# Performance work log

Measured on AMD Instinct MI355X. Metric: run time of the kernel, lower is better.

## Reference

```python
import jax, jax.numpy as jnp
import numpy as np

H = 1024
B, LK, LQ = 16, 2048, 64


def setup_inputs() -> dict:
    key0 = jax.random.key(0)
    ks = jax.random.split(key0, 16)
    f = jax.random.normal
    return {
        "query": f(ks[0], (B, 1, H), jnp.float32),
        "key": f(ks[1], (B, LK, 2 * H), jnp.float32),
        "value": f(ks[2], (B, LK, 2 * H), jnp.float32),
        "mask": jax.random.randint(ks[3], (B, 1, LK), 0, 2).astype(jnp.int32),
        "q_key": f(ks[4], (B, LQ, 2 * H), jnp.float32),
        "q_value": f(ks[5], (B, LQ, 2 * H), jnp.float32),
        "q_mask": jax.random.randint(ks[6], (B, 1, LQ), 0, 2).astype(jnp.int32),
        "alphas_state": jax.random.uniform(ks[7], (B, 1, LK), jnp.float32),
        "q_alphas_state": jax.random.uniform(ks[8], (B, 1, LQ), jnp.float32),
        # nn.Linear params: W is [out, in], y = x @ W.T + b
        "W_q": f(ks[9], (2 * H, H + 2 * H + 1), jnp.float32) * 0.02,
        "b_q": jnp.zeros((2 * H,), jnp.float32),
        "W_t": f(ks[10], (2 * H, H + 2 * H + 1 + 2 * H), jnp.float32) * 0.02,
        "b_t": jnp.zeros((2 * H,), jnp.float32),
        "query_other": jax.random.uniform(ks[11], (1, 2 * H), jnp.float32, minval=-0.005, maxval=0.005),
        "text_other": jax.random.uniform(ks[12], (1, 2 * H), jnp.float32, minval=-0.005, maxval=0.005),
    }


def reference(query, key, value, mask, q_key, q_value, q_mask,
              alphas_state, q_alphas_state,
              W_q, b_q, W_t, b_t, query_other, text_other):
    neg_inf = jnp.float32(-jnp.inf)
    Bq, Lq, _ = q_key.shape
    Bk, Lk, _ = key.shape
    # ---- query-side additive attention ----
    qrep = jnp.broadcast_to(query, (Bq, Lq, query.shape[-1]))            # repeat(1, Lq, 1)
    feat = jnp.concatenate([q_key, qrep, q_alphas_state.reshape(Bq, Lq, 1)], axis=-1)
    h = jnp.tanh(jnp.einsum('bli,oi->blo', feat, W_q) + b_q)             # [B, Lq, 2H]
    scores = jnp.einsum('blo,o->bl', h, query_other[0])[:, None, :]      # fused per-batch loop -> [B,1,Lq]
    scores = jnp.where(q_mask == 0, neg_inf, scores)
    q_alphas = jax.nn.softmax(scores, axis=-1)
    query_loss = jnp.sum(jnp.min(
        jnp.concatenate([q_alphas_state[:, 0, :], q_alphas[:, 0, :]], axis=0), axis=0))
    q_context = jnp.einsum('bql,bld->bqd', q_alphas, q_value)            # bmm -> [B,1,2H]
    # ---- text-side additive attention ----
    qrep_k = jnp.broadcast_to(query, (Bk, Lk, query.shape[-1]))
    ctx_rep = jnp.broadcast_to(q_context, (Bk, Lk, q_context.shape[-1]))
    feat_t = jnp.concatenate([key, qrep_k, alphas_state.reshape(Bk, Lk, 1), ctx_rep], axis=-1)
    h_t = jnp.tanh(jnp.einsum('bli,oi->blo', feat_t, W_t) + b_t)         # [B, Lk, 2H]
    scores_t = jnp.einsum('blo,o->bl', h_t, text_other[0])[:, None, :]   # [B,1,Lk]
    scores_t = jnp.where(mask == 0, neg_inf, scores_t)
    alphas = jax.nn.softmax(scores_t, axis=-1)
    text_loss = jnp.sum(jnp.min(
        jnp.concatenate([alphas_state[:, 0, :], alphas[:, 0, :]], axis=0), axis=0))
    context = jnp.einsum('bql,bld->bqd', alphas, value)                  # [B,1,2H]
    return (context, alphas, q_alphas, text_loss, query_loss)
```

## Files before the change

### kernel.cpp

```cpp
#include <hip/hip_runtime.h>
#include <hip/hip_bf16.h>
#include <math.h>

#define GK 2048
#define NCB 16

typedef __attribute__((ext_vector_type(8))) short bf16x8;
typedef __attribute__((ext_vector_type(4))) float f32x4;
typedef __attribute__((ext_vector_type(4))) float f4v;
typedef __attribute__((ext_vector_type(4))) unsigned short u16x4;
typedef __attribute__((ext_vector_type(8))) unsigned short u16x8;

__device__ __forceinline__ unsigned short f2bf(float x) {
    unsigned int u = __float_as_uint(x);
    u += 0x7fffu + ((u >> 16) & 1u);
    return (unsigned short)(u >> 16);
}

__device__ __forceinline__ void gl_lds16(const void* g, void* l) {
    __builtin_amdgcn_global_load_lds(
        (const __attribute__((address_space(1))) unsigned int*)g,
        (__attribute__((address_space(3))) unsigned int*)l, 16, 0, 0);
}

__global__ void prep_kernel(const float* __restrict__ Wt, const float* __restrict__ Wq,
                            const float* __restrict__ q_key, const float* __restrict__ key,
                            const float* __restrict__ query, const float* __restrict__ b_q,
                            unsigned short* __restrict__ Wtk, unsigned short* __restrict__ Wqk,
                            unsigned short* __restrict__ qkb, unsigned short* __restrict__ keyb,
                            float* __restrict__ w3q, float* __restrict__ w3t,
                            float* __restrict__ Dq) {
    int b = blockIdx.x, tid = threadIdx.x;
    if (b < 32768) {
        long i = ((long)b << 11) + (tid << 3);
        f4v a = *(const f4v*)(key + i);
        f4v c = *(const f4v*)(key + i + 4);
        u16x8 r;
        r[0] = f2bf(a[0]); r[1] = f2bf(a[1]); r[2] = f2bf(a[2]); r[3] = f2bf(a[3]);
        r[4] = f2bf(c[0]); r[5] = f2bf(c[1]); r[6] = f2bf(c[2]); r[7] = f2bf(c[3]);
        *(u16x8*)(keyb + i) = r;
        return;
    }
    int b2 = b - 32768;
    if (b2 < 2048) {
        const float* s = Wt + (size_t)b2 * 5121;
        unsigned short* d = Wtk + (size_t)b2 * 2048;
#pragma unroll
        for (int k = 0; k < 8; k++) { int c = tid + (k << 8); d[c] = f2bf(s[c]); }
    } else if (b2 < 4096) {
        int o = b2 - 2048;
        const float* s = Wq + (size_t)o * 3073;
        unsigned short* d = Wqk + (size_t)o * 2048;
#pragma unroll
        for (int k = 0; k < 8; k++) { int c = tid + (k << 8); d[c] = f2bf(s[c]); }
    } else if (b2 < 5120) {
        long i = ((long)(b2 - 4096) * 256 + tid) * 8;
        f4v a = *(const f4v*)(q_key + i);
        f4v c = *(const f4v*)(q_key + i + 4);
        u16x8 r;
        r[0] = f2bf(a[0]); r[1] = f2bf(a[1]); r[2] = f2bf(a[2]); r[3] = f2bf(a[3]);
        r[4] = f2bf(c[0]); r[5] = f2bf(c[1]); r[6] = f2bf(c[2]); r[7] = f2bf(c[3]);
        *(u16x8*)(qkb + i) = r;
    } else if (b2 < 5128) {
        int o = (b2 - 5120) * 256 + tid;
        w3q[o] = Wq[(size_t)o * 3073 + 3072];
        w3t[o] = Wt[(size_t)o * 5121 + 3072];
    } else {
        int wave = tid >> 6, lane = tid & 63;
        int o = (b2 - 5128) * 4 + wave;
        const float* wrow = Wq + (size_t)o * 3073 + 2048;
        float acc[16];
#pragma unroll
        for (int z = 0; z < 16; z++) acc[z] = 0.f;
        for (int i = lane; i < 1024; i += 64) {
            float wv = wrow[i];
            const float* qp = query + i;
#pragma unroll
            for (int z = 0; z < 16; z++) acc[z] += wv * qp[z * 1024];
        }
#pragma unroll
        for (int z = 0; z < 16; z++) {
            float v = acc[z];
            for (int off = 1; off < 64; off <<= 1) v += __shfl_xor(v, off);
            if (lane == 0) Dq[(z << 11) + o] = v + b_q[o];
        }
    }
}

template <int KLEN>
__global__ __launch_bounds__(256) void dconst_kernel(
    const float* __restrict__ W, long ldw,
    const float* __restrict__ bias,
    const float* __restrict__ query,
    const float* __restrict__ qctx,
    float* __restrict__ Dout) {
    int tid = threadIdx.x;
    int wave = tid >> 6, lane = tid & 63;
    int o = blockIdx.x * 4 + wave;
    const float* wrow = W + (size_t)o * ldw + 2048;
    float acc[16];
#pragma unroll
    for (int b2 = 0; b2 < 16; b2++) acc[b2] = 0.f;
    for (int i = lane; i < KLEN; i += 64) {
        if (KLEN == 1024 || i < 1024) {
            float wv = wrow[i];
            const float* qp = query + i;
#pragma unroll
            for (int b2 = 0; b2 < 16; b2++) acc[b2] += wv * qp[b2 * 1024];
        } else {
            float wv = wrow[i + 1];
            const float* cp = qctx + (i - 1024);
#pragma unroll
            for (int b2 = 0; b2 < 16; b2++) acc[b2] += wv * cp[b2 * 2048];
        }
    }
#pragma unroll
    for (int b2 = 0; b2 < 16; b2++) {
        float v = acc[b2];
        for (int off = 1; off < 64; off <<= 1) v += __shfl_xor(v, off);
        if (lane == 0) Dout[(b2 << 11) + o] = v + bias[o];
    }
}

template <int LOG_RPB>
__global__ __launch_bounds__(256) void gemm_score(
    const unsigned short* __restrict__ A,
    const unsigned short* __restrict__ Bt,
    const float* __restrict__ Dc,
    const float* __restrict__ avec,
    const float* __restrict__ w3,
    const float* __restrict__ tvec,
    float* __restrict__ partial,
    int row0) {
    __shared__ unsigned short As[128 * 32];
    __shared__ unsigned short Bs[128 * 32];
    __shared__ float red[128][2];

    int nwg = gridDim.x;
    int bid = blockIdx.x;
    int q8 = nwg >> 3;
    int wg = (bid & 7) * q8 + (bid >> 3);
    int rb = wg >> 4, cb = wg & 15;

    int tid = threadIdx.x;
    int wave = tid >> 6, lane = tid & 63;
    int wr = wave >> 1, wc = wave & 1;
    int l15 = lane & 15, lhi = lane >> 4;

    const unsigned short* Ab = A + (size_t)rb * 128 * GK;
    const unsigned short* Bb = Bt + (size_t)cb * 128 * GK;

    int r0 = tid >> 2, c0 = (tid & 3) << 3;

    f32x4 acc[4][4];
#pragma unroll
    for (int i = 0; i < 4; i++)
#pragma unroll
        for (int j = 0; j < 4; j++) acc[i][j] = (f32x4)0.f;

    unsigned short* AsW0 = As + (wave << 9);
    unsigned short* AsW1 = As + 2048 + (wave << 9);
    unsigned short* BsW0 = Bs + (wave << 9);
    unsigned short* BsW1 = Bs + 2048 + (wave << 9);

    for (int k0 = 0; k0 < GK; k0 += 32) {
        __syncthreads();
        gl_lds16(Ab + (size_t)r0 * GK + k0 + c0, AsW0);
        gl_lds16(Ab + (size_t)(r0 + 64) * GK + k0 + c0, AsW1);
        gl_lds16(Bb + (size_t)r0 * GK + k0 + c0, BsW0);
        gl_lds16(Bb + (size_t)(r0 + 64) * GK + k0 + c0, BsW1);
        __syncthreads();
        bf16x8 a[4], b[4];
#pragma unroll
        for (int mi = 0; mi < 4; mi++)
            a[mi] = *(const bf16x8*)(As + (((wr << 6) + (mi << 4) + l15) << 5) + (lhi << 3));
#pragma unroll
        for (int ni = 0; ni < 4; ni++)
            b[ni] = *(const bf16x8*)(Bs + (((wc << 6) + (ni << 4) + l15) << 5) + (lhi << 3));
#pragma unroll
        for (int mi = 0; mi < 4; mi++)
#pragma unroll
            for (int ni = 0; ni < 4; ni++)
                acc[mi][ni] = __builtin_amdgcn_mfma_f32_16x16x32_bf16(a[mi], b[ni], acc[mi][ni], 0, 0, 0);
    }

    int grow_base = row0 + (rb << 7) + (wr << 6);
    int bb = grow_base >> LOG_RPB;
    int gcol = (cb << 7) + (wc << 6) + l15;
    float Dco[4], w3o[4], tv[4];
#pragma unroll
    for (int ni = 0; ni < 4; ni++) {
        int o = gcol + (ni << 4);
        Dco[ni] = Dc[(bb << 11) + o];
        w3o[ni] = w3[o];
        tv[ni] = tvec[o];
    }
#pragma unroll
    for (int mi = 0; mi < 4; mi++) {
#pragma unroll
        for (int j = 0; j < 4; j++) {
            int rloc = (mi << 4) + (lhi << 2) + j;
            float av = avec[grow_base + rloc];
            float s = 0.f;
#pragma unroll
            for (int ni = 0; ni < 4; ni++) {
                float x = acc[mi][ni][j] + Dco[ni] + av * w3o[ni];
                x = fminf(fmaxf(x, -15.f), 15.f);
                float e = __expf(2.f * x);
                s += ((e - 1.f) / (e + 1.f)) * tv[ni];
            }
#pragma unroll
            for (int off = 1; off < 16; off <<= 1) s += __shfl_xor(s, off);
            if (l15 == 0) red[(wr << 6) + rloc][wc] = s;
        }
    }
    __syncthreads();
    if (tid < 128) {
        partial[(size_t)(row0 + (rb << 7) + tid) * NCB + cb] = red[tid][0] + red[tid][1];
    }
}

#define MFMA16(A, B, C) __builtin_amdgcn_mfma_f32_16x16x32_bf16(A, B, C, 0, 0, 0)

#define STAGE2(GB, GR0, K0, LB) do { \
    int _rr = lane >> 3; \
    int _cc = ((lane & 7) ^ _rr) << 3; \
    gl_lds16((GB) + (size_t)((GR0) + (wid << 3) + _rr) * GK + (K0) + _cc, lds + (LB) + (wid << 9)); \
    gl_lds16((GB) + (size_t)((GR0) + 64 + (wid << 3) + _rr) * GK + (K0) + _cc, lds + (LB) + 4096 + (wid << 9)); \
  } while (0)

#define WAIT4 do { asm volatile("s_waitcnt vmcnt(4)" ::: "memory"); __builtin_amdgcn_sched_barrier(0); } while (0)
#define NOWAIT do { } while (0)

#define PHASE(YOFF, Q, FIRSTB, STAGE_STMT, BOUNDARY) do { \
    bf16x8 a00, a01, a10, a11; \
    if (FIRSTB) { \
        b00 = *(const bf16x8*)(lds8 + bB0[0] + (YOFF)); b01 = *(const bf16x8*)(lds8 + bB1[0] + (YOFF)); \
        b10 = *(const bf16x8*)(lds8 + bB0[1] + (YOFF)); b11 = *(const bf16x8*)(lds8 + bB1[1] + (YOFF)); \
        b20 = *(const bf16x8*)(lds8 + bB0[2] + (YOFF)); b21 = *(const bf16x8*)(lds8 + bB1[2] + (YOFF)); \
        b30 = *(const bf16x8*)(lds8 + bB0[3] + (YOFF)); b31 = *(const bf16x8*)(lds8 + bB1[3] + (YOFF)); \
    } \
    a00 = *(const bf16x8*)(lds8 + aA0[2*(Q)  ] + (YOFF)); a01 = *(const bf16x8*)(lds8 + aA1[2*(Q)  ] + (YOFF)); \
    a10 = *(const bf16x8*)(lds8 + aA0[2*(Q)+1] + (YOFF)); a11 = *(const bf16x8*)(lds8 + aA1[2*(Q)+1] + (YOFF)); \
    STAGE_STMT; \
    BOUNDARY; \
    __builtin_amdgcn_s_barrier(); \
    asm volatile("s_waitcnt lgkmcnt(0)" ::: "memory"); \
    __builtin_amdgcn_sched_barrier(0); \
    __builtin_amdgcn_s_setprio(1); \
    acc[2*(Q)  ][0] = MFMA16(a00, b00, acc[2*(Q)  ][0]); \
    acc[2*(Q)  ][0] = MFMA16(a01, b01, acc[2*(Q)  ][0]); \
    acc[2*(Q)  ][1] = MFMA16(a00, b10, acc[2*(Q)  ][1]); \
    acc[2*(Q)  ][1] = MFMA16(a01, b11, acc[2*(Q)  ][1]); \
    acc[2*(Q)  ][2] = MFMA16(a00, b20, acc[2*(Q)  ][2]); \
    acc[2*(Q)  ][2] = MFMA16(a01, b21, acc[2*(Q)  ][2]); \
    acc[2*(Q)  ][3] = MFMA16(a00, b30, acc[2*(Q)  ][3]); \
    acc[2*(Q)  ][3] = MFMA16(a01, b31, acc[2*(Q)  ][3]); \
    acc[2*(Q)+1][0] = MFMA16(a10, b00, acc[2*(Q)+1][0]); \
    acc[2*(Q)+1][0] = MFMA16(a11, b01, acc[2*(Q)+1][0]); \
    acc[2*(Q)+1][1] = MFMA16(a10, b10, acc[2*(Q)+1][1]); \
    acc[2*(Q)+1][1] = MFMA16(a11, b11, acc[2*(Q)+1][1]); \
    acc[2*(Q)+1][2] = MFMA16(a10, b20, acc[2*(Q)+1][2]); \
    acc[2*(Q)+1][2] = MFMA16(a11, b21, acc[2*(Q)+1][2]); \
    acc[2*(Q)+1][3] = MFMA16(a10, b30, acc[2*(Q)+1][3]); \
    acc[2*(Q)+1][3] = MFMA16(a11, b31, acc[2*(Q)+1][3]); \
    __builtin_amdgcn_s_setprio(0); \
  } while (0)

__global__ __launch_bounds__(512, 2) void gemm256(
    const unsigned short* __restrict__ A,
    const unsigned short* __restrict__ Bt,
    const float* __restrict__ Dc,
    const float* __restrict__ avec,
    const float* __restrict__ w3,
    const float* __restrict__ tvec,
    float* __restrict__ partial) {
    extern __shared__ unsigned short lds[];
    char* lds8 = (char*)lds;
    const int XA = 0, YA = 16384, XB = 32768, YB = 49152;

    int nwg = gridDim.x;
    int bid = blockIdx.x;
    int q8 = nwg >> 3;
    int wg = (bid & 7) * q8 + (bid >> 3);
    int rb = wg >> 3, cb = wg & 7;

    int tid = threadIdx.x;
    int wid = tid >> 6, lane = tid & 63;
    int wr = wid >> 2, wc = wid & 3;
    int l15 = lane & 15, lhi = lane >> 4;

    const unsigned short* Aq = A;
    const unsigned short* Bq = Bt;
    int arow = rb << 8;
    int brow = cb << 8;

    int sw0 = ((lhi ^ (l15 & 7)) << 4);
    int sw1 = (((4 | lhi) ^ (l15 & 7)) << 4);
    int aA0[8], aA1[8], bB0[4], bB1[4];
#pragma unroll
    for (int mi = 0; mi < 8; mi++) {
        int r = (wr << 7) + (mi << 4) + l15;
        aA0[mi] = (r << 7) + sw0;
        aA1[mi] = (r << 7) + sw1;
    }
#pragma unroll
    for (int ni = 0; ni < 4; ni++) {
        int r = (wc << 6) + (ni << 4) + l15;
        bB0[ni] = 65536 + (r << 7) + sw0;
        bB1[ni] = 65536 + (r << 7) + sw1;
    }

    f32x4 acc[8][4];
#pragma unroll
    for (int i = 0; i < 8; i++)
#pragma unroll
        for (int j = 0; j < 4; j++) acc[i][j] = (f32x4)0.f;

    bf16x8 b00, b01, b10, b11, b20, b21, b30, b31;

    STAGE2(Bq, brow, 0, XB);
    STAGE2(Bq, brow + 128, 0, XB + 8192);
    STAGE2(Aq, arow, 0, XA);
    STAGE2(Aq, arow + 128, 0, XA + 8192);
    STAGE2(Bq, brow, 64, YB);
    STAGE2(Bq, brow + 128, 64, YB + 8192);
    asm volatile("s_waitcnt vmcnt(4)" ::: "memory");
    __builtin_amdgcn_sched_barrier(0);
    __builtin_amdgcn_s_barrier();

    for (int it = 0; it < 16; ++it) {
        int k1 = ((it << 1) + 1) << 6;
        int k2 = (((it << 1) + 2) << 6) & 2047;
        int k3 = (((it << 1) + 3) << 6) & 2047;
        PHASE(0,     0, 1, STAGE2(Aq, arow,       k1, YA),        NOWAIT);
        PHASE(0,     1, 0, STAGE2(Aq, arow + 128, k1, YA + 8192), NOWAIT);
        PHASE(0,     2, 0, STAGE2(Bq, brow,       k2, XB),        NOWAIT);
        PHASE(0,     3, 0, STAGE2(Bq, brow + 128, k2, XB + 8192), WAIT4);
        PHASE(32768, 0, 1, STAGE2(Aq, arow,       k2, XA),        NOWAIT);
        PHASE(32768, 1, 0, STAGE2(Aq, arow + 128, k2, XA + 8192), NOWAIT);
        PHASE(32768, 2, 0, STAGE2(Bq, brow,       k3, YB),        NOWAIT);
        PHASE(32768, 3, 0, STAGE2(Bq, brow + 128, k3, YB + 8192), WAIT4);
    }

    int gcolb = (cb << 8) + (wc << 6) + l15;
    int bb = rb >> 3;
    float Dco[4], w3o[4], tv[4];
#pragma unroll
    for (int ni = 0; ni < 4; ++ni) {
        int o = gcolb + (ni << 4);
        Dco[ni] = Dc[(bb << 11) + o];
        w3o[ni] = w3[o];
        tv[ni] = tvec[o];
    }
    float* red = (float*)(lds + 65536);
#pragma unroll
    for (int mi = 0; mi < 8; ++mi) {
#pragma unroll
        for (int j = 0; j < 4; ++j) {
            int rloc = (wr << 7) + (mi << 4) + (lhi << 2) + j;
            float av = avec[(rb << 8) + rloc];
            float s = 0.f;
#pragma unroll
            for (int ni = 0; ni < 4; ++ni) {
                float x = acc[mi][ni][j] + Dco[ni] + av * w3o[ni];
                x = fminf(fmaxf(x, -15.f), 15.f);
                float e = __expf(2.f * x);
                s += ((e - 1.f) / (e + 1.f)) * tv[ni];
            }
#pragma unroll
            for (int off2 = 1; off2 < 16; off2 <<= 1) s += __shfl_xor(s, off2);
            if (l15 == 0) red[(rloc << 2) + wc] = s;
        }
    }
    __syncthreads();
    if (tid < 256) {
        partial[(size_t)((rb << 8) + tid) * 8 + cb] =
            red[(tid << 2)] + red[(tid << 2) + 1] + red[(tid << 2) + 2] + red[(tid << 2) + 3];
    }
}

__global__ __launch_bounds__(256) void qctx_kernel(
    const float* __restrict__ partial_q, const int* __restrict__ q_mask,
    const float* __restrict__ q_value,
    float* __restrict__ out_qalphas, float* __restrict__ qctx) {
    int b = blockIdx.x, dc = blockIdx.y, tid = threadIdx.x;
    __shared__ float sal[64];
    if (tid < 64) {
        float s = 0.f;
        const float* p = partial_q + (size_t)(b * 64 + tid) * NCB;
#pragma unroll
        for (int c = 0; c < 16; c++) s += p[c];
        if (q_mask[b * 64 + tid] == 0) s = -INFINITY;
        float m = s;
        for (int off = 1; off < 64; off <<= 1) m = fmaxf(m, __shfl_xor(m, off));
        float e = (s == -INFINITY) ? 0.f : __expf(s - m);
        float sum = e;
        for (int off = 1; off < 64; off <<= 1) sum += __shfl_xor(sum, off);
        float a = e / sum;
        sal[tid] = a;
        if (dc == 0) out_qalphas[b * 64 + tid] = a;
    }
    __syncthreads();
    int d = (dc << 8) + tid;
    float acc = 0.f;
    for (int l = 0; l < 64; l++) {
        float al = sal[l];
        if (al != 0.f) acc += al * q_value[((size_t)(b * 64 + l) << 11) + d];
    }
    qctx[(b << 11) + d] = acc;
}

__global__ __launch_bounds__(256) void softmax_t_kernel(
    const float* __restrict__ partial,
    const int* __restrict__ mask,
    float* __restrict__ out_alphas) {
    int b = blockIdx.x, tid = threadIdx.x;
    int wave = tid >> 6, lane = tid & 63;
    __shared__ float sred[4];
    float sc[8];
    float lm = -INFINITY;
#pragma unroll
    for (int i = 0; i < 8; i++) {
        int l = tid + (i << 8);
        const float* p = partial + (size_t)(b * 2048 + l) * 8;
        float s = 0.f;
#pragma unroll
        for (int c = 0; c < 8; c++) s += p[c];
        if (mask[b * 2048 + l] == 0) s = -INFINITY;
        sc[i] = s;
        lm = fmaxf(lm, s);
    }
    for (int off = 1; off < 64; off <<= 1) lm = fmaxf(lm, __shfl_xor(lm, off));
    if (lane == 0) sred[wave] = lm;
    __syncthreads();
    float m = fmaxf(fmaxf(sred[0], sred[1]), fmaxf(sred[2], sred[3]));
    float ee[8];
    float ls = 0.f;
#pragma unroll
    for (int i = 0; i < 8; i++) {
        ee[i] = (sc[i] == -INFINITY) ? 0.f : __expf(sc[i] - m);
        ls += ee[i];
    }
    for (int off = 1; off < 64; off <<= 1) ls += __shfl_xor(ls, off);
    __syncthreads();
    if (lane == 0) sred[wave] = ls;
    __syncthreads();
    float S = sred[0] + sred[1] + sred[2] + sred[3];
    float inv = 1.f / S;
#pragma unroll
    for (int i = 0; i < 8; i++)
        out_alphas[b * 2048 + tid + (i << 8)] = ee[i] * inv;
}

__global__ __launch_bounds__(256) void ctx_partial_kernel(
    const float* __restrict__ alphas,
    const float* __restrict__ value,
    float* __restrict__ pctx) {
    int b = blockIdx.x, lc = blockIdx.y, tid = threadIdx.x;
    __shared__ float sa[64];
    if (tid < 64) sa[tid] = alphas[(b << 11) + (lc << 6) + tid];
    __syncthreads();
    f4v a0 = (f4v)0.f, a1 = (f4v)0.f;
    const float* vb = value + ((size_t)((b << 11) + (lc << 6)) << 11);
    for (int l = 0; l < 64; l++) {
        float al = sa[l];
        if (al != 0.f) {
            const f4v* vr = (const f4v*)(vb + ((size_t)l << 11));
            a0 += al * vr[tid];
            a1 += al * vr[tid + 256];
        }
    }
    f4v* p = (f4v*)(pctx + ((size_t)((b << 5) + lc) << 11));
    p[tid] = a0;
    p[tid + 256] = a1;
}

__global__ __launch_bounds__(256) void ctx_reduce_kernel(
    const float* __restrict__ pctx, float* __restrict__ out_ctx) {
    int b = blockIdx.x, half = blockIdx.y, tid = threadIdx.x;
    int d4 = (half << 8) + tid;
    f4v s = (f4v)0.f;
#pragma unroll
    for (int lc = 0; lc < 32; lc++)
        s += ((const f4v*)(pctx + ((size_t)((b << 5) + lc) << 11)))[d4];
    ((f4v*)(out_ctx + ((size_t)b << 11)))[d4] = s;
}

__global__ void loss_part_kernel(const float* __restrict__ qs, const float* __restrict__ qa,
                                 const float* __restrict__ ts, const float* __restrict__ ta,
                                 float* __restrict__ parts) {
    int blk = blockIdx.x, tid = threadIdx.x;
    int wave = tid >> 6, lane = tid & 63;
    __shared__ float sred[2];
    float s = 0.f;
    if (blk == 0) {
        if (tid < 64) {
            float m = INFINITY;
#pragma unroll
            for (int b = 0; b < 16; ++b) {
                m = fminf(m, qs[(b << 6) + tid]);
                m = fminf(m, qa[(b << 6) + tid]);
            }
            s = m;
        }
    } else {
        int l = ((blk - 1) << 7) + tid;
        float m = INFINITY;
#pragma unroll
        for (int b = 0; b < 16; ++b) {
            m = fminf(m, ts[(b << 11) + l]);
            m = fminf(m, ta[(b << 11) + l]);
        }
        s = m;
    }
    for (int off = 1; off < 64; off <<= 1) s += __shfl_xor(s, off);
    if (lane == 0) sred[wave] = s;
    __syncthreads();
    if (tid == 0) parts[blk] = sred[0] + sred[1];
}

__global__ void loss_final_kernel(const float* __restrict__ parts,
                                  float* __restrict__ out_tl, float* __restrict__ out_ql) {
    if (threadIdx.x == 0) {
        *out_ql = parts[0];
        float t = 0.f;
        for (int i = 1; i <= 16; ++i) t += parts[i];
        *out_tl = t;
    }
}

extern "C" void kernel_launch(void* const* d_in, const int* in_sizes, int n_in,
                              void* d_out, int out_size, void* d_ws, size_t ws_size,
                              hipStream_t stream) {
    const float* query          = (const float*)d_in[0];
    const float* key            = (const float*)d_in[1];
    const float* value          = (const float*)d_in[2];
    const int*   mask           = (const int*)d_in[3];
    const float* q_key          = (const float*)d_in[4];
    const float* q_value        = (const float*)d_in[5];
    const int*   q_mask         = (const int*)d_in[6];
    const float* alphas_state   = (const float*)d_in[7];
    const float* q_alphas_state = (const float*)d_in[8];
    const float* W_q            = (const float*)d_in[9];
    const float* b_q            = (const float*)d_in[10];
    const float* W_t            = (const float*)d_in[11];
    const float* b_t            = (const float*)d_in[12];
    const float* query_other    = (const float*)d_in[13];
    const float* text_other     = (const float*)d_in[14];

    float* out        = (float*)d_out;
    float* out_ctx     = out;
    float* out_alphas  = out + 32768;
    float* out_qalphas = out + 65536;
    float* out_tloss   = out + 66560;
    float* out_qloss   = out + 66561;

    char* w = (char*)d_ws;
    size_t off = 0;
    auto alloc = [&](size_t bytes) -> char* {
        char* p = w + off;
        off += (bytes + 255) & ~(size_t)255;
        return p;
    };
    unsigned short* Wtk  = (unsigned short*)alloc(2048ull * 2048 * 2);
    unsigned short* Wqk  = (unsigned short*)alloc(2048ull * 2048 * 2);
    unsigned short* qkb  = (unsigned short*)alloc(1024ull * 2048 * 2);
    unsigned short* keyb = (unsigned short*)alloc(32768ull * 2048 * 2);
    float* partial_t     = (float*)alloc(32768ull * 8 * 4);
    float* partial_q     = (float*)alloc(1024ull * NCB * 4);
    float* Dq            = (float*)alloc(16 * 2048 * 4);
    float* Dt            = (float*)alloc(16 * 2048 * 4);
    float* qctx          = (float*)alloc(16 * 2048 * 4);
    float* w3q           = (float*)alloc(2048 * 4);
    float* w3t           = (float*)alloc(2048 * 4);
    float* pctx          = (float*)alloc(16ull * 32 * 2048 * 4);
    float* lparts        = (float*)alloc(32 * 4);

    hipFuncSetAttribute((const void*)gemm256,
                        hipFuncAttributeMaxDynamicSharedMemorySize, 135168);

    prep_kernel<<<38408, 256, 0, stream>>>(W_t, W_q, q_key, key, query, b_q,
                                           Wtk, Wqk, qkb, keyb, w3q, w3t, Dq);

    gemm_score<6><<<128, 256, 0, stream>>>(qkb, Wqk, Dq, q_alphas_state, w3q,
                                           query_other, partial_q, 0);
    qctx_kernel<<<dim3(16, 8), 256, 0, stream>>>(partial_q, q_mask, q_value,
                                                 out_qalphas, qctx);

    dconst_kernel<3072><<<512, 256, 0, stream>>>(W_t, 5121, b_t, query, qctx, Dt);
    gemm256<<<1024, 512, 135168, stream>>>(keyb, Wtk, Dt, alphas_state, w3t,
                                           text_other, partial_t);

    softmax_t_kernel<<<16, 256, 0, stream>>>(partial_t, mask, out_alphas);
    ctx_partial_kernel<<<dim3(16, 32), 256, 0, stream>>>(out_alphas, value, pctx);
    ctx_reduce_kernel<<<dim3(16, 2), 256, 0, stream>>>(pctx, out_ctx);
    loss_part_kernel<<<17, 128, 0, stream>>>(q_alphas_state, out_qalphas,
                                             alphas_state, out_alphas, lparts);
    loss_final_kernel<<<1, 64, 0, stream>>>(lparts, out_tloss, out_qloss);
}
```

Baseline: 482.2 us.

## Compact unmasked key rows and skip masked tiles in text GEMM

A new scan kernel builds, per batch, a compacted list of unmasked key positions and their count. The bf16 key conversion gathers only those rows (zero-padded to a 256 multiple), and the text-side GEMM exits early for row tiles past the count. The softmax then scatters results back to the original positions. This aims to skip GEMM and conversion work for masked keys, which is about half with random masks, at the cost of an extra kernel launch and gather/scatter indirection.

```diff
diff --git a/kernel.cpp b/kernel.cpp
--- a/kernel.cpp
+++ b/kernel.cpp
@@ -23,22 +23,67 @@
         (__attribute__((address_space(3))) unsigned int*)l, 16, 0, 0);
 }
 
+__global__ void mask_scan_kernel(const int* __restrict__ mask,
+                                 int* __restrict__ idx, int* __restrict__ cnt) {
+    int b = blockIdx.x, tid = threadIdx.x;
+    int wave = tid >> 6, lane = tid & 63;
+    __shared__ int wsum[4];
+    __shared__ int sbase;
+    if (tid == 0) sbase = 0;
+    __syncthreads();
+    for (int c = 0; c < 8; ++c) {
+        int l = (c << 8) + tid;
+        int m = mask[(b << 11) + l];
+        unsigned long long bal = __ballot(m != 0);
+        int wpfx = __popcll(bal & ((1ull << lane) - 1ull));
+        if (lane == 0) wsum[wave] = __popcll(bal);
+        int rbase = sbase;
+        __syncthreads();
+        int woff = 0;
+#pragma unroll
+        for (int w2 = 0; w2 < 4; ++w2) if (w2 < wave) woff += wsum[w2];
+        if (m) idx[(b << 11) + rbase + woff + wpfx] = l;
+        int tot = wsum[0] + wsum[1] + wsum[2] + wsum[3];
+        __syncthreads();
+        if (tid == 0) sbase = rbase + tot;
+        __syncthreads();
+    }
+    if (tid == 0) cnt[b] = sbase;
+}
+
 __global__ void prep_kernel(const float* __restrict__ Wt, const float* __restrict__ Wq,
                             const float* __restrict__ q_key, const float* __restrict__ key,
                             const float* __restrict__ query, const float* __restrict__ b_q,
+                            const float* __restrict__ alphas_state,
+                            const int* __restrict__ idx, const int* __restrict__ cnt,
                             unsigned short* __restrict__ Wtk, unsigned short* __restrict__ Wqk,
                             unsigned short* __restrict__ qkb, unsigned short* __restrict__ keyb,
+                            float* __restrict__ avec_c,
                             float* __restrict__ w3q, float* __restrict__ w3t,
                             float* __restrict__ Dq) {
     int b = blockIdx.x, tid = threadIdx.x;
     if (b < 32768) {
-        long i = ((long)b << 11) + (tid << 3);
-        f4v a = *(const f4v*)(key + i);
-        f4v c = *(const f4v*)(key + i + 4);
-        u16x8 r;
-        r[0] = f2bf(a[0]); r[1] = f2bf(a[1]); r[2] = f2bf(a[2]); r[3] = f2bf(a[3]);
-        r[4] = f2bf(c[0]); r[5] = f2bf(c[1]); r[6] = f2bf(c[2]); r[7] = f2bf(c[3]);
-        *(u16x8*)(keyb + i) = r;
+        int bb = b >> 11, j = b & 2047;
+        int c_ = cnt[bb];
+        int lim = (c_ + 255) & ~255;
+        if (j >= lim) return;
+        unsigned short* drow = keyb + ((long)b << 11);
+        if (j < c_) {
+            int l = idx[b];
+            const float* srow = key + (((size_t)(bb << 11) + l) << 11);
+            long i = (long)tid << 3;
+            f4v a = *(const f4v*)(srow + i);
+            f4v c = *(const f4v*)(srow + i + 4);
+            u16x8 r;
+            r[0] = f2bf(a[0]); r[1] = f2bf(a[1]); r[2] = f2bf(a[2]); r[3] = f2bf(a[3]);
+            r[4] = f2bf(c[0]); r[5] = f2bf(c[1]); r[6] = f2bf(c[2]); r[7] = f2bf(c[3]);
+            *(u16x8*)(drow + i) = r;
+            if (tid == 0) avec_c[b] = alphas_state[(bb << 11) + l];
+        } else {
+            u16x8 z = (u16x8)(short)0;
+            *(u16x8*)(drow + (tid << 3)) = z;
+            if (tid == 0) avec_c[b] = 0.f;
+        }
         return;
     }
     int b2 = b - 32768;
@@ -274,6 +319,7 @@
     const float* __restrict__ avec,
     const float* __restrict__ w3,
     const float* __restrict__ tvec,
+    const int* __restrict__ cnt,
     float* __restrict__ partial) {
     extern __shared__ unsigned short lds[];
     char* lds8 = (char*)lds;
@@ -284,6 +330,8 @@
     int q8 = nwg >> 3;
     int wg = (bid & 7) * q8 + (bid >> 3);
     int rb = wg >> 3, cb = wg & 7;
+
+    if (((rb & 7) << 8) >= cnt[rb >> 3]) return;
 
     int tid = threadIdx.x;
     int wid = tid >> 6, lane = tid & 63;
@@ -413,21 +461,25 @@
 
 __global__ __launch_bounds__(256) void softmax_t_kernel(
     const float* __restrict__ partial,
-    const int* __restrict__ mask,
+    const int* __restrict__ idx, const int* __restrict__ cnt,
     float* __restrict__ out_alphas) {
     int b = blockIdx.x, tid = threadIdx.x;
     int wave = tid >> 6, lane = tid & 63;
+    int cnt_b = cnt[b];
     __shared__ float sred[4];
+#pragma unroll
+    for (int i = 0; i < 8; i++) out_alphas[(b << 11) + tid + (i << 8)] = 0.f;
+    __syncthreads();
     float sc[8];
     float lm = -INFINITY;
 #pragma unroll
     for (int i = 0; i < 8; i++) {
-        int l = tid + (i << 8);
-        const float* p = partial + (size_t)(b * 2048 + l) * 8;
+        int j = tid + (i << 8);
+        const float* p = partial + (size_t)((b << 11) + j) * 8;
         float s = 0.f;
 #pragma unroll
         for (int c = 0; c < 8; c++) s += p[c];
-        if (mask[b * 2048 + l] == 0) s = -INFINITY;
+        if (j >= cnt_b) s = -INFINITY;
         sc[i] = s;
         lm = fmaxf(lm, s);
     }
@@ -449,8 +501,11 @@
     float S = sred[0] + sred[1] + sred[2] + sred[3];
     float inv = 1.f / S;
 #pragma unroll
-    for (int i = 0; i < 8; i++)
-        out_alphas[b * 2048 + tid + (i << 8)] = ee[i] * inv;
+    for (int i = 0; i < 8; i++) {
+        int j = tid + (i << 8);
+        if (j < cnt_b)
+            out_alphas[(b << 11) + idx[(b << 11) + j]] = ee[i] * inv;
+    }
 }
 
 __global__ __launch_bounds__(256) void ctx_partial_kernel(
@@ -576,12 +631,17 @@
     float* w3t           = (float*)alloc(2048 * 4);
     float* pctx          = (float*)alloc(16ull * 32 * 2048 * 4);
     float* lparts        = (float*)alloc(32 * 4);
+    int*   idx           = (int*)alloc(32768 * 4);
+    int*   cnt           = (int*)alloc(64 * 4);
+    float* avec_c        = (float*)alloc(32768 * 4);
 
     hipFuncSetAttribute((const void*)gemm256,
                         hipFuncAttributeMaxDynamicSharedMemorySize, 135168);
 
+    mask_scan_kernel<<<16, 256, 0, stream>>>(mask, idx, cnt);
     prep_kernel<<<38408, 256, 0, stream>>>(W_t, W_q, q_key, key, query, b_q,
-                                           Wtk, Wqk, qkb, keyb, w3q, w3t, Dq);
+                                           alphas_state, idx, cnt,
+                                           Wtk, Wqk, qkb, keyb, avec_c, w3q, w3t, Dq);
 
     gemm_score<6><<<128, 256, 0, stream>>>(qkb, Wqk, Dq, q_alphas_state, w3q,
                                            query_other, partial_q, 0);
@@ -589,10 +649,10 @@
                                                  out_qalphas, qctx);
 
     dconst_kernel<3072><<<512, 256, 0, stream>>>(W_t, 5121, b_t, query, qctx, Dt);
-    gemm256<<<1024, 512, 135168, stream>>>(keyb, Wtk, Dt, alphas_state, w3t,
-                                           text_other, partial_t);
-
-    softmax_t_kernel<<<16, 256, 0, stream>>>(partial_t, mask, out_alphas);
+    gemm256<<<1024, 512, 135168, stream>>>(keyb, Wtk, Dt, avec_c, w3t,
+                                           text_other, cnt, partial_t);
+
+    softmax_t_kernel<<<16, 256, 0, stream>>>(partial_t, idx, cnt, out_alphas);
     ctx_partial_kernel<<<dim3(16, 32), 256, 0, stream>>>(out_alphas, value, pctx);
     ctx_reduce_kernel<<<dim3(16, 2), 256, 0, stream>>>(pctx, out_ctx);
     loss_part_kernel<<<17, 128, 0, stream>>>(q_alphas_state, out_qalphas,
```

Result: faster. 390.5 us, median of 2 (-19.0%).
